# Performance work log

Hardware: AMD Instinct MI355X
Metric: run time of the kernel (lower is better)

The kernel has to match this reference:

```python
import jax, jax.numpy as jnp
import numpy as np

SEQ = 4096
D_EMB = 2048
D_HEAD = 128
SCALE = 0.02


def setup_inputs() -> dict:
    key = jax.random.key(0)
    kx, kq, kk, kv, ko = jax.random.split(key, 5)
    x = jax.random.normal(kx, (SEQ, D_EMB), dtype=jnp.float32)
    W_Q = jax.random.normal(kq, (D_EMB, D_EMB), dtype=jnp.float32) * SCALE
    W_K = jax.random.normal(kk, (D_EMB, D_EMB), dtype=jnp.float32) * SCALE
    W_V = jax.random.normal(kv, (D_EMB, D_EMB), dtype=jnp.float32) * SCALE
    W_O = jax.random.normal(ko, (D_EMB, D_EMB), dtype=jnp.float32) * SCALE
    b_Q = jnp.zeros((D_EMB,), dtype=jnp.float32)
    b_K = jnp.zeros((D_EMB,), dtype=jnp.float32)
    b_V = jnp.zeros((D_EMB,), dtype=jnp.float32)
    b_O = jnp.zeros((D_EMB,), dtype=jnp.float32)
    return {"x": x, "W_Q": W_Q, "W_K": W_K, "W_V": W_V, "W_O": W_O,
            "b_Q": b_Q, "b_K": b_K, "b_V": b_V, "b_O": b_O, "d_head": D_HEAD}


def reference(x, W_Q, W_K, W_V, W_O, b_Q, b_K, b_V, b_O, d_head):
    # x: [S, D]
    q = x @ W_Q + b_Q  # [S, D]
    k = x @ W_K + b_K
    v = x @ W_V + b_V
    scores = (q @ k.T) / jnp.sqrt(jnp.float32(d_head))  # [S, S]
    seq = scores.shape[0]
    causal = jnp.tril(jnp.ones((seq, seq), dtype=bool))
    scores = jnp.where(causal, scores, -jnp.inf)
    weights = jax.nn.softmax(scores, axis=-1)  # [S, S]
    attn_out = weights @ v  # [S, D]
    return attn_out @ W_O + b_O
```

## Files before the change

kernel.cpp:

```cpp
#include <hip/hip_runtime.h>
#include <hip/hip_fp16.h>

typedef _Float16 f16;
typedef _Float16 f16x8 __attribute__((ext_vector_type(8)));
typedef _Float16 f16x4 __attribute__((ext_vector_type(4)));
typedef float    f32x4 __attribute__((ext_vector_type(4)));

#define SEQ      4096
#define DEMB     2048
#define SCALE_QK 0.08838834764831845f

#define GAS __attribute__((address_space(1)))
#define LAS __attribute__((address_space(3)))

__device__ __forceinline__ void load_lds16(const f16* g, f16* l) {
    __builtin_amdgcn_global_load_lds((const GAS void*)g, (LAS void*)l, 16, 0, 0);
}

__device__ __forceinline__ f16x8 ldsr(const f16* base, int byteoff) {
    byteoff ^= (byteoff >> 3) & 0x70;
    return *(const f16x8*)((const char*)base + byteoff);
}

__device__ __forceinline__ void stage_half(const f16* __restrict__ src, int ldk,
                                           f16* ldsdst, int tid) {
#pragma unroll
    for (int s = 0; s < 2; ++s) {
        const int o   = s * 8192 + tid * 16;
        const int osw = o ^ ((o >> 3) & 0x70);
        load_lds16(src + (size_t)(osw >> 7) * ldk + ((osw & 127) >> 1),
                   ldsdst + (s * 8192 + (tid >> 6) * 1024) / 2);
    }
}

template <int MODE>
__device__ __forceinline__ void gemm_core(
        const f16* __restrict__ A, int lda, const f16* __restrict__ BT, int ldb,
        void* __restrict__ outp, int ldo, const float* __restrict__ bias,
        int bm, int bn, int NI, int kt0, float scale, f16* lds, bool excl) {
    const int m0 = bm * 256, n0 = bn * 256;

    const int tid  = threadIdx.x;
    const int lane = tid & 63;
    const int wr   = (tid >> 6) >> 2;
    const int wc   = (tid >> 6) & 3;
    const int fr   = lane & 15;
    const int kb   = (lane >> 4) * 16;

    const f16* Abase = A + (size_t)m0 * lda + kt0 * 64;
    const f16* Bbase = BT + (size_t)n0 * ldb + kt0 * 64;

#define STG(buf, isB, half, t) \
    stage_half((isB) ? (Bbase + (size_t)((half) * 128) * ldb + (t) * 64) \
                     : (Abase + (size_t)((half) * 128) * lda + (t) * 64), \
               (isB) ? ldb : lda, \
               lds + (buf) * 32768 + (isB) * 16384 + (half) * 8192, tid)

    f32x4 acc[8][4] = {};
    f16x8 af[8], bf0[4], bf1[4];

#define READ_A(Mh, buf) { \
    const f16* bb = lds + (buf) * 32768; \
    _Pragma("unroll") for (int m = 0; m < 4; ++m) \
    _Pragma("unroll") for (int ks = 0; ks < 2; ++ks) \
        af[m * 2 + ks] = ldsr(bb, ((Mh) * 128 + wr * 64 + m * 16 + fr) * 128 + ks * 64 + kb); }

#define READ_B(Nh, buf, dst) { \
    const f16* bb = lds + (buf) * 32768 + 16384; \
    _Pragma("unroll") for (int n = 0; n < 2; ++n) \
    _Pragma("unroll") for (int ks = 0; ks < 2; ++ks) \
        dst[n * 2 + ks] = ldsr(bb, ((Nh) * 128 + wc * 32 + n * 16 + fr) * 128 + ks * 64 + kb); }

#define MFMA_PH(Mh, Nh, bfx) { \
    __builtin_amdgcn_s_setprio(1); \
    _Pragma("unroll") for (int m = 0; m < 4; ++m) \
    _Pragma("unroll") for (int n = 0; n < 2; ++n) \
    _Pragma("unroll") for (int ks = 0; ks < 2; ++ks) \
        acc[(Mh) * 4 + m][(Nh) * 2 + n] = __builtin_amdgcn_mfma_f32_16x16x32_f16( \
            af[m * 2 + ks], bfx[n * 2 + ks], acc[(Mh) * 4 + m][(Nh) * 2 + n], 0, 0, 0); \
    __builtin_amdgcn_s_setprio(0); }

#define BAR   asm volatile("s_barrier" ::: "memory")
#define VM6   asm volatile("s_waitcnt vmcnt(6)" ::: "memory")
#define VM0   asm volatile("s_waitcnt vmcnt(0)" ::: "memory")

    STG(0, 0, 0, 0); STG(0, 1, 0, 0); STG(0, 1, 1, 0); STG(0, 0, 1, 0);
    STG(1, 0, 0, 1); STG(1, 1, 0, 1); STG(1, 1, 1, 1);
    VM6; BAR;

    for (int i = 0; i < NI; ++i) {
        const int t0 = 2 * i;
        const bool more = (i + 1 < NI);
        READ_A(0, 0); READ_B(0, 0, bf0);
        STG(1, 0, 1, t0 + 1);
        BAR; MFMA_PH(0, 0, bf0); BAR;
        READ_B(1, 0, bf1);
        if (more) STG(0, 0, 0, t0 + 2);
        BAR; MFMA_PH(0, 1, bf1); BAR;
        READ_A(1, 0);
        if (more) STG(0, 1, 0, t0 + 2);
        BAR; MFMA_PH(1, 0, bf0); BAR;
        if (more) { STG(0, 1, 1, t0 + 2); VM6; } else { VM0; }
        BAR; MFMA_PH(1, 1, bf1); BAR;
        READ_A(0, 1); READ_B(0, 1, bf0);
        if (more) STG(0, 0, 1, t0 + 2);
        BAR; MFMA_PH(0, 0, bf0); BAR;
        READ_B(1, 1, bf1);
        if (more) STG(1, 0, 0, t0 + 3);
        BAR; MFMA_PH(0, 1, bf1); BAR;
        READ_A(1, 1);
        if (more) STG(1, 1, 0, t0 + 3);
        BAR; MFMA_PH(1, 0, bf0); BAR;
        if (more) STG(1, 1, 1, t0 + 3);
        VM6;
        BAR; MFMA_PH(1, 1, bf1); BAR;
    }

    const int rq = (lane >> 4) * 4;
#pragma unroll
    for (int mi = 0; mi < 8; ++mi) {
        const int row = m0 + (mi >> 2) * 128 + wr * 64 + (mi & 3) * 16 + rq;
#pragma unroll
        for (int ni = 0; ni < 4; ++ni) {
            const int col = n0 + (ni >> 1) * 128 + wc * 32 + (ni & 1) * 16 + fr;
            if (MODE == 0) {
                f16* o = (f16*)outp;
                const float bv = bias[col];
#pragma unroll
                for (int r = 0; r < 4; ++r)
                    o[(size_t)(row + r) * ldo + col] = (f16)(acc[mi][ni][r] + bv);
            } else if (MODE == 1) {
                f16* o = (f16*)outp;
                f16x4 v;
#pragma unroll
                for (int r = 0; r < 4; ++r) v[r] = (f16)acc[mi][ni][r];
                *(f16x4*)&o[(size_t)col * ldo + row] = v;
            } else if (MODE == 2) {
                float* o = (float*)outp;
                const float bv = bias ? bias[col] : 0.f;
                if (excl) {
#pragma unroll
                    for (int r = 0; r < 4; ++r)
                        o[(size_t)(row + r) * ldo + col] = acc[mi][ni][r] + bv;
                } else {
#pragma unroll
                    for (int r = 0; r < 4; ++r)
                        atomicAdd(&o[(size_t)(row + r) * ldo + col], acc[mi][ni][r] + bv);
                }
            } else {
                f16* o = (f16*)outp;
#pragma unroll
                for (int r = 0; r < 4; ++r)
                    o[(size_t)(row + r) * ldo + col] = (f16)(acc[mi][ni][r] * scale);
            }
        }
    }
#undef STG
#undef READ_A
#undef READ_B
#undef MFMA_PH
#undef BAR
#undef VM6
#undef VM0
}

__global__ __launch_bounds__(256) void cvt_f16(const float* __restrict__ in,
                                               f16* __restrict__ out, int n) {
    int i = (blockIdx.x * 256 + threadIdx.x) * 4;
    if (i >= n) return;
    float4 v = *(const float4*)&in[i];
    f16x4 o; o[0] = (f16)v.x; o[1] = (f16)v.y; o[2] = (f16)v.z; o[3] = (f16)v.w;
    *(f16x4*)&out[i] = o;
}

__global__ __launch_bounds__(256) void transpose_cvt3(
        const float* __restrict__ WQ, const float* __restrict__ WK,
        const float* __restrict__ WO,
        f16* __restrict__ wqkt, f16* __restrict__ wot) {
    __shared__ f16 tile[64][72];
    const int z = blockIdx.z;
    const float* in = z == 0 ? WQ : z == 1 ? WK : WO;
    f16* out = z == 0 ? wqkt : z == 1 ? wqkt + (size_t)DEMB * DEMB : wot;
    const int c0 = blockIdx.x * 64, r0 = blockIdx.y * 64;
    const int tx = threadIdx.x & 63, ty = threadIdx.x >> 6;
    for (int rr = ty; rr < 64; rr += 4)
        tile[tx][rr] = (f16)in[(size_t)(r0 + rr) * DEMB + c0 + tx];
    __syncthreads();
    for (int cc = ty; cc < 64; cc += 4)
        out[(size_t)(c0 + cc) * DEMB + r0 + tx] = tile[cc][tx];
}

__global__ __launch_bounds__(512, 2)
void k_mix1(const f16* __restrict__ x16, const f16* __restrict__ wqkt,
            f16* __restrict__ qk16, const float* __restrict__ bqk,
            const f16* __restrict__ wv16, const f16* __restrict__ wot,
            f16* __restrict__ wvoT, const float* __restrict__ WO,
            const float* __restrict__ bV, float* __restrict__ bc) {
    __shared__ f16 lds[65536];
    const int bid = blockIdx.x;
    if (bid < 128) {
        gemm_core<0>(x16, DEMB, wqkt, DEMB, qk16, 2 * DEMB, bqk,
                     bid >> 4, bid & 15, 16, 0, 1.f, lds, false);
    } else if (bid < 192) {
        const int w = bid - 128;
        gemm_core<1>(wv16, DEMB, wot, DEMB, wvoT, DEMB, nullptr,
                     w >> 3, w & 7, 16, 0, 1.f, lds, false);
    } else {
        const int b  = bid - 192;
        const int j0 = (b & 7) * 256;
        const int i0 = (b >> 3) * 256 + (threadIdx.x >> 8) * 128;
        const int jj = threadIdx.x & 255;
        float acc = 0.f;
        for (int i = i0; i < i0 + 128; ++i)
            acc += bV[i] * WO[(size_t)i * DEMB + j0 + jj];
        atomicAdd(&bc[j0 + jj], acc);
    }
}

__global__ __launch_bounds__(512, 2)
void k_mix2(const f16* __restrict__ x16, const f16* __restrict__ wqkt,
            f16* __restrict__ qk16, const float* __restrict__ bqk,
            const f16* __restrict__ wvoT, f16* __restrict__ vwT) {
    __shared__ f16 lds[65536];
    const int bid = blockIdx.x;
    if (bid < 128) {
        gemm_core<0>(x16, DEMB, wqkt, DEMB, qk16, 2 * DEMB, bqk,
                     8 + (bid >> 4), bid & 15, 16, 0, 1.f, lds, false);
    } else {
        const int b = bid - 128;
        gemm_core<1>(x16, DEMB, wvoT, DEMB, vwT, SEQ, nullptr,
                     b >> 3, b & 7, 16, 0, 1.f, lds, false);
    }
}

__global__ __launch_bounds__(512, 2)
void k_scores(const f16* __restrict__ qk16, f16* __restrict__ sb) {
    __shared__ f16 lds[65536];
    const int bid = blockIdx.x;
    int bm = (int)((sqrtf(8.f * bid + 1.f) - 1.f) * 0.5f);
    while ((bm + 1) * (bm + 2) / 2 <= bid) ++bm;
    while (bm * (bm + 1) / 2 > bid) --bm;
    const int bn = bid - bm * (bm + 1) / 2;
    gemm_core<3>(qk16, 2 * DEMB, qk16 + DEMB, 2 * DEMB, sb, SEQ, nullptr,
                 bm, bn, 16, 0, SCALE_QK, lds, false);
}

__global__ __launch_bounds__(256) void k_softmax(f16* __restrict__ sb) {
    __shared__ f16 srow[SEQ];
    __shared__ float red[8];
    const int i  = blockIdx.x;
    const int L  = i + 1;
    const int Lp = ((i >> 8) + 1) << 8;
    f16* row = sb + (size_t)i * SEQ;
    const int t = threadIdx.x;

    float mx = -3.0e38f;
    for (int j0 = t * 8; j0 < Lp; j0 += 2048) {
        f16x8 v = *(const f16x8*)&row[j0];
        *(f16x8*)&srow[j0] = v;
#pragma unroll
        for (int u = 0; u < 8; ++u)
            if (j0 + u < L) mx = fmaxf(mx, (float)v[u]);
    }
#pragma unroll
    for (int o = 32; o > 0; o >>= 1) mx = fmaxf(mx, __shfl_xor(mx, o));
    if ((t & 63) == 0) red[t >> 6] = mx;
    __syncthreads();
    mx = fmaxf(fmaxf(red[0], red[1]), fmaxf(red[2], red[3]));

    float sm = 0.f;
    for (int j0 = t * 8; j0 < Lp; j0 += 2048) {
        f16x8 v = *(const f16x8*)&srow[j0];
#pragma unroll
        for (int u = 0; u < 8; ++u)
            if (j0 + u < L) sm += __expf((float)v[u] - mx);
    }
#pragma unroll
    for (int o = 32; o > 0; o >>= 1) sm += __shfl_xor(sm, o);
    if ((t & 63) == 0) red[4 + (t >> 6)] = sm;
    __syncthreads();
    const float inv = 1.f / (red[4] + red[5] + red[6] + red[7]);

    for (int j0 = t * 8; j0 < Lp; j0 += 2048) {
        f16x8 v = *(const f16x8*)&srow[j0];
        f16x8 wv;
#pragma unroll
        for (int u = 0; u < 8; ++u)
            wv[u] = (j0 + u < L) ? (f16)(__expf((float)v[u] - mx) * inv) : (f16)0.f;
        *(f16x8*)&row[j0] = wv;
    }
}

__global__ __launch_bounds__(512, 2)
void k_pvw(const f16* __restrict__ sb, const f16* __restrict__ vwT,
           float* __restrict__ out, const float* __restrict__ bc) {
    __shared__ f16 lds[65536];
    static const short BMt[30] = {0,1,2,3,4,5,6,6,7,7,8,8,9,9,10,10,11,11,
                                  12,12,12,13,13,13,14,14,14,15,15,15};
    static const short KT0t[30] = {0,0,0,0,0,0,0,14,0,16,0,18,0,20,0,22,0,24,
                                   0,18,36,0,20,38,0,20,40,0,22,44};
    static const short NIt[30] = {2,4,6,8,10,12,7,7,8,8,9,9,10,10,11,11,12,12,
                                  9,9,8,10,9,9,10,10,10,11,11,10};
    const int e = blockIdx.x, bn = blockIdx.y;
    const int bm = BMt[e], kt0 = KT0t[e], ni = NIt[e];
    gemm_core<2>(sb, SEQ, vwT, SEQ, out, DEMB, kt0 == 0 ? bc : nullptr,
                 bm, bn, ni, kt0, 1.f, lds, e < 6);
}

extern "C" void kernel_launch(void* const* d_in, const int* in_sizes, int n_in,
                              void* d_out, int out_size, void* d_ws, size_t ws_size,
                              hipStream_t stream) {
    const float* x  = (const float*)d_in[0];
    const float* WQ = (const float*)d_in[1];
    const float* WK = (const float*)d_in[2];
    const float* WV = (const float*)d_in[3];
    const float* WO = (const float*)d_in[4];
    const float* bQ = (const float*)d_in[5];
    const float* bK = (const float*)d_in[6];
    const float* bV = (const float*)d_in[7];
    const float* bO = (const float*)d_in[8];
    float* out = (float*)d_out;

    char* w = (char*)d_ws;
    f16* qk16 = (f16*)w; w += (size_t)SEQ * 2 * DEMB * 2;
    f16* sb   = (f16*)w; w += (size_t)SEQ * SEQ * 2;
    f16* x16  = (f16*)w; w += (size_t)SEQ * DEMB * 2;
    f16* wqkt = (f16*)w; w += (size_t)2 * DEMB * DEMB * 2;
    f16* wv16 = (f16*)w; w += (size_t)DEMB * DEMB * 2;
    f16* wot  = (f16*)w; w += (size_t)DEMB * DEMB * 2;
    f16* wvoT = (f16*)w; w += (size_t)DEMB * DEMB * 2;
    float* bqk = (float*)w; w += 2 * DEMB * 4;
    float* bc  = (float*)w; w += DEMB * 4 + 4096;
    f16* vwT = wv16;

    cvt_f16<<<(SEQ * DEMB) / 1024, 256, 0, stream>>>(x, x16, SEQ * DEMB);
    cvt_f16<<<(DEMB * DEMB) / 1024, 256, 0, stream>>>(WV, wv16, DEMB * DEMB);
    transpose_cvt3<<<dim3(DEMB / 64, DEMB / 64, 3), 256, 0, stream>>>(
        WQ, WK, WO, wqkt, wot);
    hipMemcpyAsync(bqk, bQ, DEMB * 4, hipMemcpyDeviceToDevice, stream);
    hipMemcpyAsync(bqk + DEMB, bK, DEMB * 4, hipMemcpyDeviceToDevice, stream);
    hipMemcpyAsync(bc, bO, DEMB * 4, hipMemcpyDeviceToDevice, stream);

    k_mix1<<<256, 512, 0, stream>>>(x16, wqkt, qk16, bqk, wv16, wot, wvoT,
                                    WO, bV, bc);

    k_mix2<<<256, 512, 0, stream>>>(x16, wqkt, qk16, bqk, wvoT, vwT);

    k_scores<<<136, 512, 0, stream>>>(qk16, sb);

    k_softmax<<<SEQ, 256, 0, stream>>>(sb);

    hipMemsetAsync(out + (size_t)1536 * DEMB, 0,
                   (size_t)(SEQ - 1536) * DEMB * 4, stream);
    k_pvw<<<dim3(30, 8), 512, 0, stream>>>(sb, vwT, out, bc);
}
```

Measured before the change: 308.1 us.

## Replace split-K atomics with partial buffers and reduce kernel; fuse prep launches

The final PV×W GEMM previously split long rows across K-chunks and combined them with float atomicAdd into a zeroed output. Now the first chunk writes directly with bias, and later chunks write to separate partial buffers (reusing the qk16 workspace), which a new reduce kernel adds into the output. This removes the memset and atomic traffic at the cost of an extra launch and extra read/write passes over the partials. The two fp16 conversion kernels and three bias memcpys are also merged into one prep kernel to cut launch overhead.

```diff
diff --git a/kernel.cpp b/kernel.cpp
--- a/kernel.cpp
+++ b/kernel.cpp
@@ -37,7 +37,7 @@
 __device__ __forceinline__ void gemm_core(
         const f16* __restrict__ A, int lda, const f16* __restrict__ BT, int ldb,
         void* __restrict__ outp, int ldo, const float* __restrict__ bias,
-        int bm, int bn, int NI, int kt0, float scale, f16* lds, bool excl) {
+        int bm, int bn, int NI, int kt0, float scale, f16* lds, int roff) {
     const int m0 = bm * 256, n0 = bn * 256;
 
     const int tid  = threadIdx.x;
@@ -137,15 +137,15 @@
                 *(f16x4*)&o[(size_t)col * ldo + row] = v;
             } else if (MODE == 2) {
                 float* o = (float*)outp;
-                const float bv = bias ? bias[col] : 0.f;
-                if (excl) {
+                if (bias) {
+                    const float bv = bias[col];
 #pragma unroll
                     for (int r = 0; r < 4; ++r)
                         o[(size_t)(row + r) * ldo + col] = acc[mi][ni][r] + bv;
                 } else {
 #pragma unroll
                     for (int r = 0; r < 4; ++r)
-                        atomicAdd(&o[(size_t)(row + r) * ldo + col], acc[mi][ni][r] + bv);
+                        o[(size_t)(row - roff + r) * ldo + col] = acc[mi][ni][r];
                 }
             } else {
                 f16* o = (f16*)outp;
@@ -164,13 +164,30 @@
 #undef VM0
 }
 
-__global__ __launch_bounds__(256) void cvt_f16(const float* __restrict__ in,
-                                               f16* __restrict__ out, int n) {
-    int i = (blockIdx.x * 256 + threadIdx.x) * 4;
-    if (i >= n) return;
-    float4 v = *(const float4*)&in[i];
-    f16x4 o; o[0] = (f16)v.x; o[1] = (f16)v.y; o[2] = (f16)v.z; o[3] = (f16)v.w;
-    *(f16x4*)&out[i] = o;
+__global__ __launch_bounds__(256) void k_prep(
+        const float* __restrict__ x, const float* __restrict__ WV,
+        const float* __restrict__ bQ, const float* __restrict__ bK,
+        const float* __restrict__ bO,
+        f16* __restrict__ x16, f16* __restrict__ wv16,
+        float* __restrict__ bqk, float* __restrict__ bc) {
+    const int bid = blockIdx.x;
+    if (bid < 12288) {
+        const bool isX = bid < 8192;
+        const float* src = isX ? x : WV;
+        f16* dst = isX ? x16 : wv16;
+        const int i = (isX ? bid : bid - 8192) * 1024 + threadIdx.x * 4;
+        float4 v = *(const float4*)&src[i];
+        f16x4 o; o[0] = (f16)v.x; o[1] = (f16)v.y; o[2] = (f16)v.z; o[3] = (f16)v.w;
+        *(f16x4*)&dst[i] = o;
+    } else if (bid < 12292) {
+        const int i = (bid - 12288) * 1024 + threadIdx.x * 4;
+        float4 v = (i < 2048) ? *(const float4*)&bQ[i]
+                              : *(const float4*)&bK[i - 2048];
+        *(float4*)&bqk[i] = v;
+    } else {
+        const int i = (bid - 12292) * 1024 + threadIdx.x * 4;
+        *(float4*)&bc[i] = *(const float4*)&bO[i];
+    }
 }
 
 __global__ __launch_bounds__(256) void transpose_cvt3(
@@ -200,11 +217,11 @@
     const int bid = blockIdx.x;
     if (bid < 128) {
         gemm_core<0>(x16, DEMB, wqkt, DEMB, qk16, 2 * DEMB, bqk,
-                     bid >> 4, bid & 15, 16, 0, 1.f, lds, false);
+                     bid >> 4, bid & 15, 16, 0, 1.f, lds, 0);
     } else if (bid < 192) {
         const int w = bid - 128;
         gemm_core<1>(wv16, DEMB, wot, DEMB, wvoT, DEMB, nullptr,
-                     w >> 3, w & 7, 16, 0, 1.f, lds, false);
+                     w >> 3, w & 7, 16, 0, 1.f, lds, 0);
     } else {
         const int b  = bid - 192;
         const int j0 = (b & 7) * 256;
@@ -225,11 +242,11 @@
     const int bid = blockIdx.x;
     if (bid < 128) {
         gemm_core<0>(x16, DEMB, wqkt, DEMB, qk16, 2 * DEMB, bqk,
-                     8 + (bid >> 4), bid & 15, 16, 0, 1.f, lds, false);
+                     8 + (bid >> 4), bid & 15, 16, 0, 1.f, lds, 0);
     } else {
         const int b = bid - 128;
         gemm_core<1>(x16, DEMB, wvoT, DEMB, vwT, SEQ, nullptr,
-                     b >> 3, b & 7, 16, 0, 1.f, lds, false);
+                     b >> 3, b & 7, 16, 0, 1.f, lds, 0);
     }
 }
 
@@ -242,7 +259,7 @@
     while (bm * (bm + 1) / 2 > bid) --bm;
     const int bn = bid - bm * (bm + 1) / 2;
     gemm_core<3>(qk16, 2 * DEMB, qk16 + DEMB, 2 * DEMB, sb, SEQ, nullptr,
-                 bm, bn, 16, 0, SCALE_QK, lds, false);
+                 bm, bn, 16, 0, SCALE_QK, lds, 0);
 }
 
 __global__ __launch_bounds__(256) void k_softmax(f16* __restrict__ sb) {
@@ -293,7 +310,8 @@
 
 __global__ __launch_bounds__(512, 2)
 void k_pvw(const f16* __restrict__ sb, const f16* __restrict__ vwT,
-           float* __restrict__ out, const float* __restrict__ bc) {
+           float* __restrict__ out, const float* __restrict__ bc,
+           float* __restrict__ part1, float* __restrict__ part2) {
     __shared__ f16 lds[65536];
     static const short BMt[30] = {0,1,2,3,4,5,6,6,7,7,8,8,9,9,10,10,11,11,
                                   12,12,12,13,13,13,14,14,14,15,15,15};
@@ -301,10 +319,28 @@
                                    0,18,36,0,20,38,0,20,40,0,22,44};
     static const short NIt[30] = {2,4,6,8,10,12,7,7,8,8,9,9,10,10,11,11,12,12,
                                   9,9,8,10,9,9,10,10,10,11,11,10};
+    static const short ORDt[30] = {0,0,0,0,0,0,0,1,0,1,0,1,0,1,0,1,0,1,
+                                   0,1,2,0,1,2,0,1,2,0,1,2};
     const int e = blockIdx.x, bn = blockIdx.y;
-    const int bm = BMt[e], kt0 = KT0t[e], ni = NIt[e];
-    gemm_core<2>(sb, SEQ, vwT, SEQ, out, DEMB, kt0 == 0 ? bc : nullptr,
-                 bm, bn, ni, kt0, 1.f, lds, e < 6);
+    const int bm = BMt[e], kt0 = KT0t[e], ni = NIt[e], ord = ORDt[e];
+    float* op = ord == 0 ? out : ord == 1 ? part1 : part2;
+    const int roff = ord == 1 ? 1536 : 3072;
+    gemm_core<2>(sb, SEQ, vwT, SEQ, op, DEMB, ord == 0 ? bc : nullptr,
+                 bm, bn, ni, kt0, 1.f, lds, roff);
+}
+
+__global__ __launch_bounds__(256) void k_reduce(
+        float* __restrict__ out, const float* __restrict__ part1,
+        const float* __restrict__ part2) {
+    const int idx = (blockIdx.x * 256 + threadIdx.x) * 4;
+    float4 o = *(float4*)&out[(size_t)1536 * DEMB + idx];
+    float4 p = *(const float4*)&part1[idx];
+    o.x += p.x; o.y += p.y; o.z += p.z; o.w += p.w;
+    if (idx >= 1536 * DEMB) {
+        float4 q = *(const float4*)&part2[idx - 1536 * DEMB];
+        o.x += q.x; o.y += q.y; o.z += q.z; o.w += q.w;
+    }
+    *(float4*)&out[(size_t)1536 * DEMB + idx] = o;
 }
 
 extern "C" void kernel_launch(void* const* d_in, const int* in_sizes, int n_in,
@@ -332,14 +368,12 @@
     float* bqk = (float*)w; w += 2 * DEMB * 4;
     float* bc  = (float*)w; w += DEMB * 4 + 4096;
     f16* vwT = wv16;
-
-    cvt_f16<<<(SEQ * DEMB) / 1024, 256, 0, stream>>>(x, x16, SEQ * DEMB);
-    cvt_f16<<<(DEMB * DEMB) / 1024, 256, 0, stream>>>(WV, wv16, DEMB * DEMB);
+    float* part1 = (float*)qk16;
+    float* part2 = (float*)qk16 + (size_t)2560 * DEMB;
+
+    k_prep<<<12294, 256, 0, stream>>>(x, WV, bQ, bK, bO, x16, wv16, bqk, bc);
     transpose_cvt3<<<dim3(DEMB / 64, DEMB / 64, 3), 256, 0, stream>>>(
         WQ, WK, WO, wqkt, wot);
-    hipMemcpyAsync(bqk, bQ, DEMB * 4, hipMemcpyDeviceToDevice, stream);
-    hipMemcpyAsync(bqk + DEMB, bK, DEMB * 4, hipMemcpyDeviceToDevice, stream);
-    hipMemcpyAsync(bc, bO, DEMB * 4, hipMemcpyDeviceToDevice, stream);
 
     k_mix1<<<256, 512, 0, stream>>>(x16, wqkt, qk16, bqk, wv16, wot, wvoT,
                                     WO, bV, bc);
@@ -350,7 +384,7 @@
 
     k_softmax<<<SEQ, 256, 0, stream>>>(sb);
 
-    hipMemsetAsync(out + (size_t)1536 * DEMB, 0,
-                   (size_t)(SEQ - 1536) * DEMB * 4, stream);
-    k_pvw<<<dim3(30, 8), 512, 0, stream>>>(sb, vwT, out, bc);
-}
+    k_pvw<<<dim3(30, 8), 512, 0, stream>>>(sb, vwT, out, bc, part1, part2);
+
+    k_reduce<<<5120, 256, 0, stream>>>(out, part1, part2);
+}
```

Result: faster. 286.4 us (-7.1%).
